# Optimization experiments

Hardware: AMD Instinct MI355X
Metric: run time of the kernel (lower is better)

The kernel has to match this reference:

```python
import jax, jax.numpy as jnp
import numpy as np

EMBED_DIM = 2048
NUM_HEADS = 32
NUM_KV_HEADS = 8
HEAD_DIM = EMBED_DIM // NUM_HEADS  # 64
KV_DIM = HEAD_DIM * NUM_KV_HEADS   # 512
Q_PER_KV = NUM_HEADS // NUM_KV_HEADS  # 4


def setup_inputs() -> dict:
    key = jax.random.key(0)
    ks = jax.random.split(key, 9)
    s = 1.0 / np.sqrt(EMBED_DIM)
    x = jax.random.normal(ks[0], (2, 2048, EMBED_DIM), dtype=jnp.float32)
    Wq = jax.random.uniform(ks[1], (EMBED_DIM, EMBED_DIM), jnp.float32, -s, s)
    bq = jax.random.uniform(ks[2], (EMBED_DIM,), jnp.float32, -s, s)
    Wk = jax.random.uniform(ks[3], (KV_DIM, EMBED_DIM), jnp.float32, -s, s)
    bk = jax.random.uniform(ks[4], (KV_DIM,), jnp.float32, -s, s)
    Wv = jax.random.uniform(ks[5], (KV_DIM, EMBED_DIM), jnp.float32, -s, s)
    bv = jax.random.uniform(ks[6], (KV_DIM,), jnp.float32, -s, s)
    Wo = jax.random.uniform(ks[7], (EMBED_DIM, EMBED_DIM), jnp.float32, -s, s)
    bo = jax.random.uniform(ks[8], (EMBED_DIM,), jnp.float32, -s, s)
    return {"x": x, "Wq": Wq, "bq": bq, "Wk": Wk, "bk": bk,
            "Wv": Wv, "bv": bv, "Wo": Wo, "bo": bo}


def reference(x, Wq, bq, Wk, bk, Wv, bv, Wo, bo):
    B, S, E = x.shape
    # projections (torch Linear: x @ W.T + b)
    q = x @ Wq.T + bq                       # [B,S,E]
    k = x @ Wk.T + bk                       # [B,S,KV_DIM]
    v = x @ Wv.T + bv
    # [B, num_kv, q_per_kv, S, D] and [B, num_kv, S, D] -- GQA grouping
    # avoids repeat_interleave duplication while computing identical math
    q = q.reshape(B, S, NUM_KV_HEADS, Q_PER_KV, HEAD_DIM).transpose(0, 2, 3, 1, 4)
    k = k.reshape(B, S, NUM_KV_HEADS, HEAD_DIM).transpose(0, 2, 1, 3)
    v = v.reshape(B, S, NUM_KV_HEADS, HEAD_DIM).transpose(0, 2, 1, 3)
    scale = 1.0 / np.sqrt(HEAD_DIM).astype(np.float32)
    scores = jnp.einsum('bgqsd,bgtd->bgqst', q, k) * scale  # [B,G,Qpk,S,S]
    causal = jnp.triu(jnp.ones((S, S), dtype=bool), k=1)
    scores = jnp.where(causal, jnp.float32(-jnp.inf), scores)
    attn = jax.nn.softmax(scores, axis=-1)
    out = jnp.einsum('bgqst,bgtd->bgqsd', attn, v)          # [B,G,Qpk,S,D]
    # back to [B,S,E]: head order matches repeat_interleave (kv-major)
    out = out.transpose(0, 3, 1, 2, 4).reshape(B, S, E)
    return out @ Wo.T + bo
```

## Files before the change

kernel.cpp:

```cpp
#include <hip/hip_runtime.h>
#include <stdint.h>

#define EMBED  2048
#define SEQ    2048
#define BATCH  2
#define NHEADS 32
#define NKV    8
#define HDIM   64
#define KVD    512
#define MTOT   (BATCH*SEQ)
#define QKVN   (EMBED + 2*KVD)

typedef __bf16 bf16x8 __attribute__((ext_vector_type(8)));
typedef float  f32x4  __attribute__((ext_vector_type(4)));
typedef float  f32x8v __attribute__((ext_vector_type(8)));
typedef float  f32x2v __attribute__((ext_vector_type(2)));
typedef float  f32x16 __attribute__((ext_vector_type(16)));

#define QSCALE 0.18033688f
#define M2     11.541560f

static __device__ __forceinline__ unsigned short f2bf(float f) {
    union { float f; unsigned int u; } v; v.f = f;
    return (unsigned short)((v.u + 0x7fffu + ((v.u >> 16) & 1u)) >> 16);
}

static __device__ __forceinline__ void gload_lds16(const void* g, void* l) {
    __builtin_amdgcn_global_load_lds(
        (const __attribute__((address_space(1))) void*)g,
        (__attribute__((address_space(3))) void*)l, 16, 0, 0);
}

template<int N> static __device__ __forceinline__ void waitvm() {
    if constexpr (N == 2) asm volatile("s_waitcnt vmcnt(2)" ::: "memory");
    else if constexpr (N == 3) asm volatile("s_waitcnt vmcnt(3)" ::: "memory");
    else if constexpr (N == 5) asm volatile("s_waitcnt vmcnt(5)" ::: "memory");
    else asm volatile("s_waitcnt vmcnt(4)" ::: "memory");
}

static __device__ __forceinline__ void cast4(const float* __restrict__ in,
                                             unsigned short* __restrict__ out, int i) {
    float4 f = reinterpret_cast<const float4*>(in)[i];
    ushort4 o;
    o.x = f2bf(f.x); o.y = f2bf(f.y); o.z = f2bf(f.z); o.w = f2bf(f.w);
    reinterpret_cast<ushort4*>(out)[i] = o;
}

__global__ __launch_bounds__(256)
void prep(const float* __restrict__ x,  const float* __restrict__ Wq,
          const float* __restrict__ Wk, const float* __restrict__ Wv,
          const float* __restrict__ Wo, const float* __restrict__ bq,
          const float* __restrict__ bk, const float* __restrict__ bv,
          unsigned short* __restrict__ xb, unsigned short* __restrict__ Wqkvb,
          unsigned short* __restrict__ Wob, float* __restrict__ bqkv)
{
    const int t0 = blockIdx.x * blockDim.x + threadIdx.x;
    const int st = gridDim.x * blockDim.x;
    for (int i = t0; i < (MTOT * EMBED) / 4;  i += st) cast4(x,  xb, i);
    for (int i = t0; i < (EMBED * EMBED) / 4; i += st) cast4(Wq, Wqkvb, i);
    for (int i = t0; i < (KVD * EMBED) / 4;   i += st) cast4(Wk, Wqkvb + EMBED * EMBED, i);
    for (int i = t0; i < (KVD * EMBED) / 4;   i += st) cast4(Wv, Wqkvb + (EMBED + KVD) * EMBED, i);
    for (int i = t0; i < (EMBED * EMBED) / 4; i += st) cast4(Wo, Wob, i);
    if (t0 < QKVN / 4) {
        float4 v = (t0 < EMBED / 4) ? reinterpret_cast<const float4*>(bq)[t0]
                 : (t0 < (EMBED + KVD) / 4) ? reinterpret_cast<const float4*>(bk)[t0 - EMBED / 4]
                 : reinterpret_cast<const float4*>(bv)[t0 - (EMBED + KVD) / 4];
        reinterpret_cast<float4*>(bqkv)[t0] = v;
    }
}

__global__ __launch_bounds__(256)
void transpose_v(const unsigned short* __restrict__ qkv,
                 unsigned short* __restrict__ vt)
{
    __shared__ __align__(16) unsigned short T[64][72];
    const int bg = blockIdx.x & 15;
    const int bt = blockIdx.x >> 4;
    const int b  = bg >> 3, g = bg & 7;
    const int tid = threadIdx.x;
    const int tr  = tid >> 2, c = tid & 3;

    const unsigned short* src = qkv + ((size_t)(b * SEQ + bt * 64 + tr)) * QKVN
                              + (EMBED + KVD) + g * HDIM + c * 16;
    uint4 v0 = *reinterpret_cast<const uint4*>(src);
    uint4 v1 = *reinterpret_cast<const uint4*>(src + 8);
    *reinterpret_cast<uint4*>(&T[tr][c * 16])     = v0;
    *reinterpret_cast<uint4*>(&T[tr][c * 16 + 8]) = v1;
    __syncthreads();

    const int dr = tr;
    unsigned short o[16];
#pragma unroll
    for (int j = 0; j < 16; ++j) o[j] = T[c * 16 + j][dr];
    unsigned short* dst = vt + ((size_t)(bg * 64 + dr)) * SEQ + bt * 64 + c * 16;
    *reinterpret_cast<uint4*>(dst)     = *reinterpret_cast<uint4*>(o);
    *reinterpret_cast<uint4*>(dst + 8) = *reinterpret_cast<uint4*>(o + 8);
}

__global__ __launch_bounds__(512, 1)
void gemm192(const unsigned short* __restrict__ A,
             const unsigned short* __restrict__ B,
             const float* __restrict__ bias,
             unsigned short* __restrict__ C, int M, int N, int K)
{
    constexpr int ASZ   = 256 * 128;
    constexpr int BSZ   = 192 * 128;
    constexpr int AHALF = ASZ / 2;
    constexpr int BUFSZ = ASZ + BSZ;

    __shared__ __align__(16) char lds[2 * BUFSZ];

    const int tid = threadIdx.x;
    const int l   = tid & 63;
    const int w   = tid >> 6;
    const int wr  = w >> 2, wc = w & 3;
    const int lr15 = l & 15;
    const int lkb  = (l >> 4) * 16;

    const int nwg = gridDim.x;
    const int cpx = nwg >> 3;
    const int bid = blockIdx.x;
    const int swz = (bid & 7) * cpx + (bid >> 3);
    const int NMB = M / 256;
    const int m0  = (swz % NMB) * 256;
    const int n0  = (swz / NMB) * 192;

    unsigned offA[2][2], dA[2][2];
#pragma unroll
    for (int q = 0; q < 2; ++q)
#pragma unroll
        for (int j = 0; j < 2; ++j) {
            int L  = q * AHALF + (tid + j * 512) * 16;
            int R  = L >> 7;
            int cb = (L & 127) ^ ((R & 7) << 4);
            int lrow = ((R >> 6) & 1) * 128 + (R >> 7) * 64 + (R & 63);
            offA[q][j] = (unsigned)((m0 + lrow) * K * 2 + cb);
            dA[q][j]   = (unsigned)L;
        }
    unsigned offB[3], dB[3];
#pragma unroll
    for (int q = 0; q < 3; ++q) {
        int L  = q * 8192 + tid * 16;
        int R  = L >> 7;
        int cb = (L & 127) ^ ((R & 7) << 4);
        offB[q] = (unsigned)((n0 + R) * K * 2 + cb);
        dB[q]   = (unsigned)(ASZ + L);
    }

#define STAGE_A(q, bw, ku) { _Pragma("unroll") \
    for (int j_ = 0; j_ < 2; ++j_) \
        gload_lds16((const char*)A + offA[q][j_] + (unsigned)(ku) * 128u, (bw) + dA[q][j_]); }
#define STAGE_B(q, bw, ku) \
    gload_lds16((const char*)B + offB[q] + (unsigned)(ku) * 128u, (bw) + dB[q]);

    auto rdA = [&](const char* br, int mi, int kk) -> bf16x8 {
        int row  = (mi >> 2) * 128 + wr * 64 + (mi & 3) * 16 + lr15;
        int byte = (row * 128 + kk * 64 + lkb) ^ ((row & 7) << 4);
        return *reinterpret_cast<const bf16x8*>(br + byte);
    };
    auto rdB = [&](const char* br, int ni, int kk) -> bf16x8 {
        int row  = ni * 64 + wc * 16 + lr15;
        int byte = (row * 128 + kk * 64 + lkb) ^ ((row & 7) << 4);
        return *reinterpret_cast<const bf16x8*>(br + ASZ + byte);
    };

    f32x4 acc[8][3] = {};
    bf16x8 afr[4][2], bf[3][2];

    STAGE_A(0, lds, 0); STAGE_B(0, lds, 0); STAGE_B(1, lds, 0);
    STAGE_B(2, lds, 0); STAGE_A(1, lds, 0);
    waitvm<4>();
    __builtin_amdgcn_s_barrier();

    const int NKT = K >> 6;
    for (int u = 0; u < NKT; ++u) {
        char* br = lds + (u & 1) * BUFSZ;
        char* bw = lds + ((u & 1) ^ 1) * BUFSZ;
        const bool pf = (u + 1 < NKT);
        const int  ku = u + 1;

        if (pf) STAGE_A(0, bw, ku);
#pragma unroll
        for (int mi = 0; mi < 4; ++mi)
#pragma unroll
            for (int kk = 0; kk < 2; ++kk) afr[mi][kk] = rdA(br, mi, kk);
#pragma unroll
        for (int kk = 0; kk < 2; ++kk) bf[0][kk] = rdB(br, 0, kk);
        __builtin_amdgcn_s_setprio(1);
#pragma unroll
        for (int mi = 0; mi < 4; ++mi)
#pragma unroll
            for (int kk = 0; kk < 2; ++kk)
                acc[mi][0] = __builtin_amdgcn_mfma_f32_16x16x32_bf16(afr[mi][kk], bf[0][kk], acc[mi][0], 0, 0, 0);
        __builtin_amdgcn_s_setprio(0);
        waitvm<5>();
        __builtin_amdgcn_s_barrier();

        if (pf) STAGE_B(0, bw, ku);
#pragma unroll
        for (int kk = 0; kk < 2; ++kk) bf[1][kk] = rdB(br, 1, kk);
        __builtin_amdgcn_s_setprio(1);
#pragma unroll
        for (int mi = 0; mi < 4; ++mi)
#pragma unroll
            for (int kk = 0; kk < 2; ++kk)
                acc[mi][1] = __builtin_amdgcn_mfma_f32_16x16x32_bf16(afr[mi][kk], bf[1][kk], acc[mi][1], 0, 0, 0);
        __builtin_amdgcn_s_setprio(0);
        waitvm<5>();
        __builtin_amdgcn_s_barrier();

        if (pf) STAGE_B(1, bw, ku);
#pragma unroll
        for (int kk = 0; kk < 2; ++kk) bf[2][kk] = rdB(br, 2, kk);
        __builtin_amdgcn_s_setprio(1);
#pragma unroll
        for (int mi = 0; mi < 4; ++mi)
#pragma unroll
            for (int kk = 0; kk < 2; ++kk)
                acc[mi][2] = __builtin_amdgcn_mfma_f32_16x16x32_bf16(afr[mi][kk], bf[2][kk], acc[mi][2], 0, 0, 0);
        __builtin_amdgcn_s_setprio(0);
        waitvm<4>();
        __builtin_amdgcn_s_barrier();

        if (pf) STAGE_B(2, bw, ku);
#pragma unroll
        for (int mi = 0; mi < 4; ++mi)
#pragma unroll
            for (int kk = 0; kk < 2; ++kk) afr[mi][kk] = rdA(br, 4 + mi, kk);
        __builtin_amdgcn_s_setprio(1);
#pragma unroll
        for (int mi = 0; mi < 4; ++mi)
#pragma unroll
            for (int kk = 0; kk < 2; ++kk)
                acc[4 + mi][0] = __builtin_amdgcn_mfma_f32_16x16x32_bf16(afr[mi][kk], bf[0][kk], acc[4 + mi][0], 0, 0, 0);
        __builtin_amdgcn_s_setprio(0);

        if (pf) STAGE_A(1, bw, ku);
        __builtin_amdgcn_s_setprio(1);
#pragma unroll
        for (int mi = 0; mi < 4; ++mi)
#pragma unroll
            for (int kk = 0; kk < 2; ++kk)
                acc[4 + mi][1] = __builtin_amdgcn_mfma_f32_16x16x32_bf16(afr[mi][kk], bf[1][kk], acc[4 + mi][1], 0, 0, 0);
        __builtin_amdgcn_s_setprio(0);

        __builtin_amdgcn_s_setprio(1);
#pragma unroll
        for (int mi = 0; mi < 4; ++mi)
#pragma unroll
            for (int kk = 0; kk < 2; ++kk)
                acc[4 + mi][2] = __builtin_amdgcn_mfma_f32_16x16x32_bf16(afr[mi][kk], bf[2][kk], acc[4 + mi][2], 0, 0, 0);
        __builtin_amdgcn_s_setprio(0);
        waitvm<4>();
        __builtin_amdgcn_s_barrier();
    }
#undef STAGE_A
#undef STAGE_B

    float bv[3];
#pragma unroll
    for (int ni = 0; ni < 3; ++ni) bv[ni] = bias[n0 + ni * 64 + wc * 16 + lr15];
#pragma unroll
    for (int mi = 0; mi < 8; ++mi)
#pragma unroll
        for (int ni = 0; ni < 3; ++ni)
#pragma unroll
            for (int r = 0; r < 4; ++r) {
                int row = m0 + wr * 128 + mi * 16 + (l >> 4) * 4 + r;
                int col = n0 + ni * 64 + wc * 16 + lr15;
                C[(size_t)row * N + col] = f2bf(acc[mi][ni][r] + bv[ni]);
            }
}

template<int WM, bool OUT_BF16>
__global__ __launch_bounds__(512, 1)
void gemm8p(const unsigned short* __restrict__ A,
            const unsigned short* __restrict__ B,
            const float* __restrict__ bias,
            void* __restrict__ C, int M, int N, int K)
{
    constexpr int BM    = WM * 32;
    constexpr int ASZ   = BM * 128;
    constexpr int BSZ   = 256 * 128;
    constexpr int AHALF = ASZ / 2;
    constexpr int AL    = AHALF / 8192;
    constexpr int BUFSZ = ASZ + BSZ;

    __shared__ __align__(16) char lds[2 * BUFSZ];

    const int tid = threadIdx.x;
    const int l   = tid & 63;
    const int w   = tid >> 6;
    const int wr  = w >> 2, wc = w & 3;
    const int lr15 = l & 15;
    const int lkb  = (l >> 4) * 16;

    const int nwg = gridDim.x;
    const int cpx = nwg >> 3;
    const int bid = blockIdx.x;
    const int swz = (bid & 7) * cpx + (bid >> 3);
    const int NMB = M / BM;
    const int m0  = (swz % NMB) * BM;
    const int n0  = (swz / NMB) * 256;

    unsigned offA[2][AL], dA[2][AL];
#pragma unroll
    for (int q = 0; q < 2; ++q)
#pragma unroll
        for (int j = 0; j < AL; ++j) {
            int L  = q * AHALF + (tid + j * 512) * 16;
            int R  = L >> 7;
            int cb = (L & 127) ^ ((R & 7) << 4);
            int lrow;
            if constexpr (WM == 8) lrow = ((R >> 6) & 1) * 128 + (R >> 7) * 64 + (R & 63);
            else                   lrow = ((R >> 5) & 1) * 64  + (R >> 6) * 32 + (R & 31);
            offA[q][j] = (unsigned)((m0 + lrow) * K * 2 + cb);
            dA[q][j]   = (unsigned)L;
        }
    unsigned offB[2][2], dB[2][2];
#pragma unroll
    for (int q = 0; q < 2; ++q)
#pragma unroll
        for (int j = 0; j < 2; ++j) {
            int L  = q * 16384 + (tid + j * 512) * 16;
            int R  = L >> 7;
            int cb = (L & 127) ^ ((R & 7) << 4);
            int lrow = ((R >> 5) & 3) * 64 + (R >> 7) * 32 + (R & 31);
            offB[q][j] = (unsigned)((n0 + lrow) * K * 2 + cb);
            dB[q][j]   = (unsigned)(ASZ + L);
        }

#define STAGE_A(q, bw, ku) { _Pragma("unroll") \
    for (int j_ = 0; j_ < AL; ++j_) \
        gload_lds16((const char*)A + offA[q][j_] + (unsigned)(ku) * 128u, (bw) + dA[q][j_]); }
#define STAGE_B(q, bw, ku) { _Pragma("unroll") \
    for (int j_ = 0; j_ < 2; ++j_) \
        gload_lds16((const char*)B + offB[q][j_] + (unsigned)(ku) * 128u, (bw) + dB[q][j_]); }

    auto rdA = [&](const char* br, int mi, int kk) -> bf16x8 {
        int row;
        if constexpr (WM == 8) row = (mi >> 2) * 128 + wr * 64 + (mi & 3) * 16 + lr15;
        else                   row = (mi >> 1) * 64  + wr * 32 + (mi & 1) * 16 + lr15;
        int byte = (row * 128 + kk * 64 + lkb) ^ ((row & 7) << 4);
        return *reinterpret_cast<const bf16x8*>(br + byte);
    };
    auto rdB = [&](const char* br, int ni, int kk) -> bf16x8 {
        int row  = (ni >> 1) * 128 + wc * 32 + (ni & 1) * 16 + lr15;
        int byte = (row * 128 + kk * 64 + lkb) ^ ((row & 7) << 4);
        return *reinterpret_cast<const bf16x8*>(br + ASZ + byte);
    };

    f32x4 acc[WM][4] = {};
    bf16x8 afr[WM / 2][2], bf0[2][2], bf1[2][2];

    STAGE_A(0, lds, 0); STAGE_B(0, lds, 0); STAGE_B(1, lds, 0); STAGE_A(1, lds, 0);
    waitvm<2 + AL>();
    __builtin_amdgcn_s_barrier();

    const int NKT = K >> 6;
    for (int u = 0; u < NKT; ++u) {
        char* br = lds + (u & 1) * BUFSZ;
        char* bw = lds + ((u & 1) ^ 1) * BUFSZ;
        const bool pf = (u + 1 < NKT);
        const int  ku = u + 1;

        if (pf) STAGE_A(0, bw, ku);
#pragma unroll
        for (int mi = 0; mi < WM / 2; ++mi)
#pragma unroll
            for (int kk = 0; kk < 2; ++kk) afr[mi][kk] = rdA(br, mi, kk);
#pragma unroll
        for (int ni = 0; ni < 2; ++ni)
#pragma unroll
            for (int kk = 0; kk < 2; ++kk) bf0[ni][kk] = rdB(br, ni, kk);
        __builtin_amdgcn_s_setprio(1);
#pragma unroll
        for (int mi = 0; mi < WM / 2; ++mi)
#pragma unroll
            for (int ni = 0; ni < 2; ++ni)
#pragma unroll
                for (int kk = 0; kk < 2; ++kk)
                    acc[mi][ni] = __builtin_amdgcn_mfma_f32_16x16x32_bf16(afr[mi][kk], bf0[ni][kk], acc[mi][ni], 0, 0, 0);
        __builtin_amdgcn_s_setprio(0);
        waitvm<2 * AL>();
        __builtin_amdgcn_s_barrier();

        if (pf) STAGE_B(0, bw, ku);
#pragma unroll
        for (int ni = 0; ni < 2; ++ni)
#pragma unroll
            for (int kk = 0; kk < 2; ++kk) bf1[ni][kk] = rdB(br, 2 + ni, kk);
        __builtin_amdgcn_s_setprio(1);
#pragma unroll
        for (int mi = 0; mi < WM / 2; ++mi)
#pragma unroll
            for (int ni = 0; ni < 2; ++ni)
#pragma unroll
                for (int kk = 0; kk < 2; ++kk)
                    acc[mi][2 + ni] = __builtin_amdgcn_mfma_f32_16x16x32_bf16(afr[mi][kk], bf1[ni][kk], acc[mi][2 + ni], 0, 0, 0);
        __builtin_amdgcn_s_setprio(0);
        waitvm<AL + 2>();
        __builtin_amdgcn_s_barrier();

        if (pf) STAGE_B(1, bw, ku);
#pragma unroll
        for (int mi = 0; mi < WM / 2; ++mi)
#pragma unroll
            for (int kk = 0; kk < 2; ++kk) afr[mi][kk] = rdA(br, WM / 2 + mi, kk);
        __builtin_amdgcn_s_setprio(1);
#pragma unroll
        for (int mi = 0; mi < WM / 2; ++mi)
#pragma unroll
            for (int ni = 0; ni < 2; ++ni)
#pragma unroll
                for (int kk = 0; kk < 2; ++kk)
                    acc[WM / 2 + mi][ni] = __builtin_amdgcn_mfma_f32_16x16x32_bf16(afr[mi][kk], bf0[ni][kk], acc[WM / 2 + mi][ni], 0, 0, 0);
        __builtin_amdgcn_s_setprio(0);

        if (pf) STAGE_A(1, bw, ku);
        __builtin_amdgcn_s_setprio(1);
#pragma unroll
        for (int mi = 0; mi < WM / 2; ++mi)
#pragma unroll
            for (int ni = 0; ni < 2; ++ni)
#pragma unroll
                for (int kk = 0; kk < 2; ++kk)
                    acc[WM / 2 + mi][2 + ni] = __builtin_amdgcn_mfma_f32_16x16x32_bf16(afr[mi][kk], bf1[ni][kk], acc[WM / 2 + mi][2 + ni], 0, 0, 0);
        __builtin_amdgcn_s_setprio(0);
        waitvm<2 + AL>();
        __builtin_amdgcn_s_barrier();
    }
#undef STAGE_A
#undef STAGE_B

    float bv[4];
#pragma unroll
    for (int ni = 0; ni < 4; ++ni) bv[ni] = bias[n0 + wc * 64 + ni * 16 + lr15];
#pragma unroll
    for (int mi = 0; mi < WM; ++mi)
#pragma unroll
        for (int ni = 0; ni < 4; ++ni)
#pragma unroll
            for (int r = 0; r < 4; ++r) {
                int row = m0 + wr * (WM * 16) + mi * 16 + (l >> 4) * 4 + r;
                int col = n0 + wc * 64 + ni * 16 + lr15;
                float v = acc[mi][ni][r] + bv[ni];
                if constexpr (OUT_BF16)
                    ((unsigned short*)C)[(size_t)row * N + col] = f2bf(v);
                else
                    ((float*)C)[(size_t)row * N + col] = v;
            }
}

static __device__ __forceinline__ bf16x8 pack_frag(float p0, float p1, float p2, float p3,
                                                   float p4, float p5, float p6, float p7) {
    unsigned int w0, w1, w2, w3;
    asm("v_cvt_pk_bf16_f32 %0, %1, %2" : "=v"(w0) : "v"(p0), "v"(p1));
    asm("v_cvt_pk_bf16_f32 %0, %1, %2" : "=v"(w1) : "v"(p2), "v"(p3));
    asm("v_cvt_pk_bf16_f32 %0, %1, %2" : "=v"(w2) : "v"(p4), "v"(p5));
    asm("v_cvt_pk_bf16_f32 %0, %1, %2" : "=v"(w3) : "v"(p6), "v"(p7));
    asm("v_permlane32_swap_b32 %0, %1" : "+v"(w0), "+v"(w2));
    asm("v_permlane32_swap_b32 %0, %1" : "+v"(w1), "+v"(w3));
    union { unsigned int u[4]; bf16x8 v; } uu;
    uu.u[0] = w0; uu.u[1] = w1; uu.u[2] = w2; uu.u[3] = w3;
    return uu.v;
}

static __device__ __forceinline__ float hsum32(f32x16 a, f32x16 b) {
    f32x16 t = a + b;
    f32x8v u = __builtin_shufflevector(t, t, 0,1,2,3,4,5,6,7)
             + __builtin_shufflevector(t, t, 8,9,10,11,12,13,14,15);
    f32x4 v4 = __builtin_shufflevector(u, u, 0,1,2,3)
             + __builtin_shufflevector(u, u, 4,5,6,7);
    f32x2v v2 = __builtin_shufflevector(v4, v4, 0,1)
              + __builtin_shufflevector(v4, v4, 2,3);
    return v2[0] + v2[1];
}

__global__ __launch_bounds__(256, 2)
void gqa_attn(const unsigned short* __restrict__ qkv,
              const unsigned short* __restrict__ vtg,
              unsigned short* __restrict__ ctx)
{
    __shared__ __align__(16) unsigned short Ks[2][64 * 64];
    __shared__ __align__(16) unsigned short Vs[2][64 * 64];

    const int bid = blockIdx.x;
    const int g   = bid & 7;
    const int bh  = (bid >> 3) & 3;
    const int b   = bh >> 1;
    const int hp  = bh & 1;
    const int qt  = 31 - (bid >> 5);
    const int NT  = qt + 1;

    const int tid = threadIdx.x;
    const int l   = tid & 63;
    const int w   = tid >> 6;
    const int hi  = l >> 5;
    const int lq  = l & 31;

    const int h   = g * 4 + hp * 2 + (w >> 1);
    const int q0  = qt * 64 + (w & 1) * 32;
    const size_t rowb = (size_t)b * SEQ;
    const int kbase = EMBED + g * HDIM;

    bf16x8 qf[4];
    {
        const char* qa = (const char*)qkv + ((rowb + q0 + lq) * QKVN + (size_t)h * HDIM) * 2;
#pragma unroll
        for (int ks = 0; ks < 4; ++ks) {
            bf16x8 ta = *reinterpret_cast<const bf16x8*>(qa + (ks * 16 + hi * 8) * 2);
#pragma unroll
            for (int j = 0; j < 8; ++j)
                ta[j] = (__bf16)((float)ta[j] * QSCALE);
            qf[ks] = ta;
        }
    }

    f32x16 acc0 = {}, acc1 = {};
    float l_run = 0.0f;

    const int Lk0 = tid << 4;
    const int Lk1 = (tid + 256) << 4;
    const int Tk0 = Lk0 ^ (((Lk0 >> 7) & 7) << 4);
    const int Tk1 = Lk1 ^ (((Lk1 >> 7) & 7) << 4);
    const int kr0 = Tk0 >> 7, ko0 = Tk0 & 127;
    const int kr1 = Tk1 >> 7, ko1 = Tk1 & 127;

    const char* vtb = (const char*)vtg + (size_t)(b * 8 + g) * HDIM * SEQ * 2;

#define STAGE_KV(buf, tt) { \
    gload_lds16((const char*)qkv + ((rowb + (tt) + kr0) * QKVN + kbase) * 2 + ko0, (char*)Ks[buf] + Lk0); \
    gload_lds16((const char*)qkv + ((rowb + (tt) + kr1) * QKVN + kbase) * 2 + ko1, (char*)Ks[buf] + Lk1); \
    gload_lds16(vtb + ((size_t)kr0 * SEQ + (tt)) * 2 + ko0, (char*)Vs[buf] + Lk0); \
    gload_lds16(vtb + ((size_t)kr1 * SEQ + (tt)) * 2 + ko1, (char*)Vs[buf] + Lk1); }

    STAGE_KV(0, 0);
    __syncthreads();

    for (int kt = 0; kt < NT; ++kt) {
        const int cur = kt & 1;
        const int t0  = kt * 64;
        const bool haveNext = (kt + 1 < NT);
        if (haveNext) STAGE_KV(cur ^ 1, t0 + 64);

        const char* KsBuf = (const char*)Ks[cur];
        f32x16 s0 = {}, s1 = {};
        __builtin_amdgcn_s_setprio(1);
#pragma unroll
        for (int ks = 0; ks < 4; ++ks) {
            const int colb = (ks * 16 + hi * 8) * 2;
            int a0 = (lq * 128 + colb) ^ ((lq & 7) << 4);
            bf16x8 kf0 = *reinterpret_cast<const bf16x8*>(KsBuf + a0);
            s0 = __builtin_amdgcn_mfma_f32_32x32x16_bf16(kf0, qf[ks], s0, 0, 0, 0);
            int r1 = 32 + lq;
            int a1 = (r1 * 128 + colb) ^ ((r1 & 7) << 4);
            bf16x8 kf1 = *reinterpret_cast<const bf16x8*>(KsBuf + a1);
            s1 = __builtin_amdgcn_mfma_f32_32x32x16_bf16(kf1, qf[ks], s1, 0, 0, 0);
        }
        __builtin_amdgcn_s_setprio(0);

        if (kt == qt) {
            const int q = q0 + lq;
#pragma unroll
            for (int r = 0; r < 16; ++r) {
                int tg = t0 + (r & 3) + 8 * (r >> 2) + 4 * hi;
                if (tg > q) s0[r] = -1e30f;
                if (tg + 32 > q) s1[r] = -1e30f;
            }
        }

        s0 = s0 - M2;
        s1 = s1 - M2;
#pragma unroll
        for (int r = 0; r < 16; ++r) {
            s0[r] = __builtin_amdgcn_exp2f(s0[r]);
            s1[r] = __builtin_amdgcn_exp2f(s1[r]);
        }

        float rs = hsum32(s0, s1);
        l_run += rs + __shfl_xor(rs, 32);

        bf16x8 pa[4];
        pa[0] = pack_frag(s0[0], s0[1], s0[2], s0[3], s0[4], s0[5], s0[6], s0[7]);
        pa[1] = pack_frag(s0[8], s0[9], s0[10], s0[11], s0[12], s0[13], s0[14], s0[15]);
        pa[2] = pack_frag(s1[0], s1[1], s1[2], s1[3], s1[4], s1[5], s1[6], s1[7]);
        pa[3] = pack_frag(s1[8], s1[9], s1[10], s1[11], s1[12], s1[13], s1[14], s1[15]);

        const char* VsBuf = (const char*)Vs[cur];
        __builtin_amdgcn_s_setprio(1);
#pragma unroll
        for (int ks = 0; ks < 4; ++ks) {
            const int colb = (ks * 16 + hi * 8) * 2;
            int a0 = (lq * 128 + colb) ^ ((lq & 7) << 4);
            bf16x8 vf0 = *reinterpret_cast<const bf16x8*>(VsBuf + a0);
            acc0 = __builtin_amdgcn_mfma_f32_32x32x16_bf16(pa[ks], vf0, acc0, 0, 0, 0);
            int d1 = 32 + lq;
            int a1 = (d1 * 128 + colb) ^ ((d1 & 7) << 4);
            bf16x8 vf1 = *reinterpret_cast<const bf16x8*>(VsBuf + a1);
            acc1 = __builtin_amdgcn_mfma_f32_32x32x16_bf16(pa[ks], vf1, acc1, 0, 0, 0);
        }
        __builtin_amdgcn_s_setprio(0);

        if (haveNext) __syncthreads();
    }
#undef STAGE_KV

#pragma unroll
    for (int r = 0; r < 16; ++r) {
        int qr  = (r & 3) + 8 * (r >> 2) + 4 * hi;
        int col = h * HDIM + lq;
        float lr = __shfl(l_run, qr);
        size_t row = rowb + q0 + qr;
        ctx[row * EMBED + col]      = f2bf(acc0[r] / lr);
        ctx[row * EMBED + col + 32] = f2bf(acc1[r] / lr);
    }
}

extern "C" void kernel_launch(void* const* d_in, const int* in_sizes, int n_in,
                              void* d_out, int out_size, void* d_ws, size_t ws_size,
                              hipStream_t stream) {
    (void)in_sizes; (void)n_in; (void)out_size; (void)ws_size;
    const float* x  = (const float*)d_in[0];
    const float* Wq = (const float*)d_in[1];
    const float* bq = (const float*)d_in[2];
    const float* Wk = (const float*)d_in[3];
    const float* bk = (const float*)d_in[4];
    const float* Wv = (const float*)d_in[5];
    const float* bv = (const float*)d_in[6];
    const float* Wo = (const float*)d_in[7];
    const float* bo = (const float*)d_in[8];
    float* out = (float*)d_out;

    char* ws = (char*)d_ws;
    unsigned short* xb    = (unsigned short*)(ws);
    unsigned short* Wqkvb = (unsigned short*)(ws + 16777216);
    unsigned short* Wob   = (unsigned short*)(ws + 29360128);
    float*          bqkv  = (float*)         (ws + 37748736);
    unsigned short* QKVb  = (unsigned short*)(ws + 37761024);
    unsigned short* ctx   = (unsigned short*)(ws + 62926848);
    unsigned short* VT    = xb;

    prep<<<2048, 256, 0, stream>>>(x, Wq, Wk, Wv, Wo, bq, bk, bv,
                                   xb, Wqkvb, Wob, bqkv);

    gemm192<<<dim3(256), 512, 0, stream>>>(
        xb, Wqkvb, bqkv, QKVb, MTOT, QKVN, EMBED);

    transpose_v<<<dim3(512), 256, 0, stream>>>(QKVb, VT);

    gqa_attn<<<dim3(1024), 256, 0, stream>>>(QKVb, VT, ctx);

    gemm8p<4, false><<<dim3(256), 512, 0, stream>>>(
        ctx, Wob, bo, out, MTOT, EMBED, EMBED);
}
```

Before: 164.6 us.

## Software-pipeline LDS fragment reads across K-iterations in QKV GEMM

```diff
diff --git a/kernel.cpp b/kernel.cpp
--- a/kernel.cpp
+++ b/kernel.cpp
@@ -165,12 +165,18 @@
     };
 
     f32x4 acc[8][3] = {};
-    bf16x8 afr[4][2], bf[3][2];
+    bf16x8 afrLo[4][2], afrHi[4][2], bf[3][2];
 
     STAGE_A(0, lds, 0); STAGE_B(0, lds, 0); STAGE_B(1, lds, 0);
     STAGE_B(2, lds, 0); STAGE_A(1, lds, 0);
-    waitvm<4>();
+    waitvm<3>();
     __builtin_amdgcn_s_barrier();
+#pragma unroll
+    for (int mi = 0; mi < 4; ++mi)
+#pragma unroll
+        for (int kk = 0; kk < 2; ++kk) afrLo[mi][kk] = rdA(lds, mi, kk);
+#pragma unroll
+    for (int kk = 0; kk < 2; ++kk) bf[0][kk] = rdB(lds, 0, kk);
 
     const int NKT = K >> 6;
     for (int u = 0; u < NKT; ++u) {
@@ -181,78 +187,78 @@
 
         if (pf) STAGE_A(0, bw, ku);
 #pragma unroll
+        for (int kk = 0; kk < 2; ++kk) bf[1][kk] = rdB(br, 1, kk);
+        __builtin_amdgcn_s_setprio(1);
+#pragma unroll
         for (int mi = 0; mi < 4; ++mi)
 #pragma unroll
-            for (int kk = 0; kk < 2; ++kk) afr[mi][kk] = rdA(br, mi, kk);
-#pragma unroll
-        for (int kk = 0; kk < 2; ++kk) bf[0][kk] = rdB(br, 0, kk);
-        __builtin_amdgcn_s_setprio(1);
-#pragma unroll
-        for (int mi = 0; mi < 4; ++mi)
-#pragma unroll
             for (int kk = 0; kk < 2; ++kk)
-                acc[mi][0] = __builtin_amdgcn_mfma_f32_16x16x32_bf16(afr[mi][kk], bf[0][kk], acc[mi][0], 0, 0, 0);
-        __builtin_amdgcn_s_setprio(0);
-        waitvm<5>();
-        __builtin_amdgcn_s_barrier();
-
-        if (pf) STAGE_B(0, bw, ku);
-#pragma unroll
-        for (int kk = 0; kk < 2; ++kk) bf[1][kk] = rdB(br, 1, kk);
-        __builtin_amdgcn_s_setprio(1);
-#pragma unroll
-        for (int mi = 0; mi < 4; ++mi)
-#pragma unroll
-            for (int kk = 0; kk < 2; ++kk)
-                acc[mi][1] = __builtin_amdgcn_mfma_f32_16x16x32_bf16(afr[mi][kk], bf[1][kk], acc[mi][1], 0, 0, 0);
-        __builtin_amdgcn_s_setprio(0);
-        waitvm<5>();
-        __builtin_amdgcn_s_barrier();
-
-        if (pf) STAGE_B(1, bw, ku);
-#pragma unroll
-        for (int kk = 0; kk < 2; ++kk) bf[2][kk] = rdB(br, 2, kk);
-        __builtin_amdgcn_s_setprio(1);
-#pragma unroll
-        for (int mi = 0; mi < 4; ++mi)
-#pragma unroll
-            for (int kk = 0; kk < 2; ++kk)
-                acc[mi][2] = __builtin_amdgcn_mfma_f32_16x16x32_bf16(afr[mi][kk], bf[2][kk], acc[mi][2], 0, 0, 0);
+                acc[mi][0] = __builtin_amdgcn_mfma_f32_16x16x32_bf16(afrLo[mi][kk], bf[0][kk], acc[mi][0], 0, 0, 0);
         __builtin_amdgcn_s_setprio(0);
         waitvm<4>();
         __builtin_amdgcn_s_barrier();
 
+        if (pf) STAGE_B(0, bw, ku);
+#pragma unroll
+        for (int kk = 0; kk < 2; ++kk) bf[2][kk] = rdB(br, 2, kk);
+        __builtin_amdgcn_s_setprio(1);
+#pragma unroll
+        for (int mi = 0; mi < 4; ++mi)
+#pragma unroll
+            for (int kk = 0; kk < 2; ++kk)
+                acc[mi][1] = __builtin_amdgcn_mfma_f32_16x16x32_bf16(afrLo[mi][kk], bf[1][kk], acc[mi][1], 0, 0, 0);
+        __builtin_amdgcn_s_setprio(0);
+        waitvm<3>();
+        __builtin_amdgcn_s_barrier();
+
+        if (pf) STAGE_B(1, bw, ku);
+#pragma unroll
+        for (int mi = 0; mi < 4; ++mi)
+#pragma unroll
+            for (int kk = 0; kk < 2; ++kk) afrHi[mi][kk] = rdA(br, 4 + mi, kk);
+        __builtin_amdgcn_s_setprio(1);
+#pragma unroll
+        for (int mi = 0; mi < 4; ++mi)
+#pragma unroll
+            for (int kk = 0; kk < 2; ++kk)
+                acc[mi][2] = __builtin_amdgcn_mfma_f32_16x16x32_bf16(afrLo[mi][kk], bf[2][kk], acc[mi][2], 0, 0, 0);
+        __builtin_amdgcn_s_setprio(0);
+
         if (pf) STAGE_B(2, bw, ku);
+        __builtin_amdgcn_s_setprio(1);
 #pragma unroll
         for (int mi = 0; mi < 4; ++mi)
 #pragma unroll
-            for (int kk = 0; kk < 2; ++kk) afr[mi][kk] = rdA(br, 4 + mi, kk);
+            for (int kk = 0; kk < 2; ++kk)
+                acc[4 + mi][0] = __builtin_amdgcn_mfma_f32_16x16x32_bf16(afrHi[mi][kk], bf[0][kk], acc[4 + mi][0], 0, 0, 0);
+        __builtin_amdgcn_s_setprio(0);
+
+        if (pf) STAGE_A(1, bw, ku);
         __builtin_amdgcn_s_setprio(1);
 #pragma unroll
         for (int mi = 0; mi < 4; ++mi)
 #pragma unroll
             for (int kk = 0; kk < 2; ++kk)
-                acc[4 + mi][0] = __builtin_amdgcn_mfma_f32_16x16x32_bf16(afr[mi][kk], bf[0][kk], acc[4 + mi][0], 0, 0, 0);
-        __builtin_amdgcn_s_setprio(0);
-
-        if (pf) STAGE_A(1, bw, ku);
+                acc[4 + mi][1] = __builtin_amdgcn_mfma_f32_16x16x32_bf16(afrHi[mi][kk], bf[1][kk], acc[4 + mi][1], 0, 0, 0);
+        __builtin_amdgcn_s_setprio(0);
+
         __builtin_amdgcn_s_setprio(1);
 #pragma unroll
         for (int mi = 0; mi < 4; ++mi)
 #pragma unroll
             for (int kk = 0; kk < 2; ++kk)
-                acc[4 + mi][1] = __builtin_amdgcn_mfma_f32_16x16x32_bf16(afr[mi][kk], bf[1][kk], acc[4 + mi][1], 0, 0, 0);
-        __builtin_amdgcn_s_setprio(0);
-
-        __builtin_amdgcn_s_setprio(1);
-#pragma unroll
-        for (int mi = 0; mi < 4; ++mi)
-#pragma unroll
-            for (int kk = 0; kk < 2; ++kk)
-                acc[4 + mi][2] = __builtin_amdgcn_mfma_f32_16x16x32_bf16(afr[mi][kk], bf[2][kk], acc[4 + mi][2], 0, 0, 0);
-        __builtin_amdgcn_s_setprio(0);
-        waitvm<4>();
+                acc[4 + mi][2] = __builtin_amdgcn_mfma_f32_16x16x32_bf16(afrHi[mi][kk], bf[2][kk], acc[4 + mi][2], 0, 0, 0);
+        __builtin_amdgcn_s_setprio(0);
+        waitvm<3>();
         __builtin_amdgcn_s_barrier();
+        if (pf) {
+#pragma unroll
+            for (int mi = 0; mi < 4; ++mi)
+#pragma unroll
+                for (int kk = 0; kk < 2; ++kk) afrLo[mi][kk] = rdA(bw, mi, kk);
+#pragma unroll
+            for (int kk = 0; kk < 2; ++kk) bf[0][kk] = rdB(bw, 0, kk);
+        }
     }
 #undef STAGE_A
 #undef STAGE_B
```

Measured after the change: 161.8 us. No clear change (-1.7%).
